# Kernel tuning notes

Measured on AMD Instinct MI355X. Metric: run time of the kernel, lower is better.

The kernel has to match this reference:

```python
import jax, jax.numpy as jnp
import numpy as np

BLOCK_N = 64  # KV tile size used by the Triton kernel (affects numerics: kernel is not exact softmax)


def _flash_fwd_buggy(q, k, v, sm_scale):
    """Faithful reproduction of the kernel's online-softmax loop.

    Note: the original kernel omits the accumulator rescaling step of true
    flash attention (acc is accumulated with the *running* denominator and
    never corrected), so we replicate that block-wise update exactly.
    q: [B,H,Sq,D], k/v: [B,H,Sk,D], Sk % BLOCK_N == 0.
    """
    B, H, Sq, D = q.shape
    Sk = k.shape[2]
    nblk = Sk // BLOCK_N
    # [nblk, B, H, BLOCK_N, D]
    kb = jnp.moveaxis(k.reshape(B, H, nblk, BLOCK_N, D), 2, 0)
    vb = jnp.moveaxis(v.reshape(B, H, nblk, BLOCK_N, D), 2, 0)

    acc0 = jnp.zeros((B, H, Sq, D), dtype=jnp.float32)
    m0 = jnp.full((B, H, Sq), -jnp.inf, dtype=jnp.float32)
    l0 = jnp.zeros((B, H, Sq), dtype=jnp.float32)

    def step(carry, kv):
        acc, m_prev, l_prev = carry
        kblk, vblk = kv  # [B,H,BLOCK_N,D]
        qk = jnp.einsum('bhmd,bhnd->bhmn', q, kblk) * sm_scale  # [B,H,Sq,BLOCK_N]
        m_curr = jnp.maximum(jnp.max(qk, axis=-1), m_prev)
        qk_exp = jnp.exp(qk - m_curr[..., None])
        l_curr = jnp.sum(qk_exp, axis=-1)
        l_new = l_prev * jnp.exp(m_prev - m_curr) + l_curr
        p = qk_exp / l_new[..., None]
        acc = acc + jnp.einsum('bhmn,bhnd->bhmd', p, vblk)
        return (acc, m_curr, l_new), None

    (acc, _, _), _ = jax.lax.scan(step, (acc0, m0, l0), (kb, vb))
    return acc


def setup_inputs() -> dict:
    key = jax.random.key(0)
    kq, kk, kv = jax.random.split(key, 3)
    B, H, S, D = 2, 16, 4096, 128
    q = jax.random.normal(kq, (B, H, S, D), dtype=jnp.float32)
    k = jax.random.normal(kk, (B, H, S, D), dtype=jnp.float32)
    v = jax.random.normal(kv, (B, H, S, D), dtype=jnp.float32)
    return {"q": q, "k": k, "v": v}


def reference(q, k, v):
    head_dim = q.shape[-1]
    sm_scale = 1.0 / np.sqrt(head_dim).astype(np.float32)
    # causal=False, dropout=0.0 (module defaults); module returns (output, None)
    return _flash_fwd_buggy(q, k, v, sm_scale)
```

## Files before the change

### kernel.cpp

```cpp
#include <hip/hip_runtime.h>
#include <hip/hip_bf16.h>
#include <math.h>


typedef __attribute__((ext_vector_type(8)))  unsigned short ushort8;
typedef __attribute__((ext_vector_type(8)))  __bf16        bf16x8;
typedef __attribute__((ext_vector_type(16))) float         f32x16;
typedef __attribute__((ext_vector_type(4)))  float         floatv4;
typedef __attribute__((ext_vector_type(2)))  unsigned int  uint2v;
typedef __attribute__((ext_vector_type(4)))  unsigned int  uint4v;

#define SQ   4096
#define SKV  4096
#define DH   128
#define BN   64
#define QB   256
#define NT   (SKV / BN)
#define KLD  136
#define VTLD 72
#define KBUF (64 * KLD)
#define VBUF (DH * VTLD)

static __device__ __forceinline__ unsigned pk2(float lo, float hi) {
    unsigned r;
    asm("v_cvt_pk_bf16_f32 %0, %1, %2" : "=v"(r) : "v"(lo), "v"(hi));
    return r;
}

__global__ __launch_bounds__(512, 2) void fa_fwd_buggy(
    const float* __restrict__ Qg, const float* __restrict__ Kg,
    const float* __restrict__ Vg, float* __restrict__ Og)
{
    __shared__ unsigned short K_lds[2 * KBUF];
    __shared__ unsigned short Vt_lds[2 * VBUF];

    const int tid  = threadIdx.x;
    const int w    = tid >> 6;
    const int lane = tid & 63;
    const int c32  = lane & 31;
    const int h    = lane >> 5;

    const int wgid  = blockIdx.x;
    const int bh    = (wgid & 7) * 4 + (wgid >> 7);
    const int qtile = (wgid >> 3) & 15;
    const int qbase = qtile * QB;
    const float qscale = 0.08838834764831845f * 1.44269504088896341f;

    const float* Qrow = Qg + ((size_t)bh * SQ + qbase + w * 32 + c32) * DH;
    ushort8 qf[8];
    #pragma unroll
    for (int ds = 0; ds < 8; ++ds) {
        floatv4 a = *(const floatv4*)(Qrow + ds * 16 + h * 8);
        floatv4 b = *(const floatv4*)(Qrow + ds * 16 + h * 8 + 4);
        uint4v u;
        u[0] = pk2(a[0]*qscale, a[1]*qscale);
        u[1] = pk2(a[2]*qscale, a[3]*qscale);
        u[2] = pk2(b[0]*qscale, b[1]*qscale);
        u[3] = pk2(b[2]*qscale, b[3]*qscale);
        qf[ds] = __builtin_bit_cast(ushort8, u);
    }

    f32x16 acc[4];
    #pragma unroll
    for (int i = 0; i < 4; ++i)
        #pragma unroll
        for (int r = 0; r < 16; ++r) acc[i][r] = 0.f;

    float l_run = 0.f;

    const float* Kbh = Kg + (size_t)bh * SKV * DH;
    const float* Vbh = Vg + (size_t)bh * SKV * DH;

    const int n_k = tid >> 3;
    const int u_k = tid & 7;
    const int dq  = tid & 31;
    const int nq  = tid >> 5;
    const int vswz = (dq >> 1) & 7;

    floatv4 ka0, ka1, kb0, kb1;
    floatv4 va0, va1, va2, va3;

#define LOAD_TILE(N0) do {                                                   \
        const float* ks_ = Kbh + (size_t)((N0) + n_k) * DH + u_k * 8;        \
        ka0 = *(const floatv4*)(ks_);        ka1 = *(const floatv4*)(ks_+4); \
        kb0 = *(const floatv4*)(ks_ + 64);   kb1 = *(const floatv4*)(ks_+68);\
        const float* vs_ = Vbh + (size_t)((N0) + nq * 4) * DH + dq * 4;      \
        va0 = *(const floatv4*)(vs_);        va1 = *(const floatv4*)(vs_+DH);\
        va2 = *(const floatv4*)(vs_+2*DH);   va3 = *(const floatv4*)(vs_+3*DH);\
    } while (0)

#define STORE_TILE(B) do {                                                   \
        unsigned short* kd_ = &K_lds[(B) * KBUF];                            \
        unsigned short* vd_ = &Vt_lds[(B) * VBUF];                           \
        uint4v u_;                                                           \
        u_[0]=pk2(ka0[0],ka0[1]); u_[1]=pk2(ka0[2],ka0[3]);                  \
        u_[2]=pk2(ka1[0],ka1[1]); u_[3]=pk2(ka1[2],ka1[3]);                  \
        *(uint4v*)&kd_[n_k * KLD + u_k * 8] = u_;                            \
        u_[0]=pk2(kb0[0],kb0[1]); u_[1]=pk2(kb0[2],kb0[3]);                  \
        u_[2]=pk2(kb1[0],kb1[1]); u_[3]=pk2(kb1[2],kb1[3]);                  \
        *(uint4v*)&kd_[n_k * KLD + (u_k + 8) * 8] = u_;                      \
        _Pragma("unroll")                                                    \
        for (int i_ = 0; i_ < 4; ++i_) {                                     \
            const int d_ = dq * 4 + i_;                                      \
            uint2v p_;                                                       \
            p_[0] = pk2(va0[i_], va1[i_]);                                   \
            p_[1] = pk2(va2[i_], va3[i_]);                                   \
            const int unit_ = (nq >> 1) ^ vswz;                              \
            *(uint2v*)&vd_[d_ * VTLD + unit_ * 8 + (nq & 1) * 4] = p_;       \
        }                                                                    \
    } while (0)

    LOAD_TILE(0);
    STORE_TILE(0);
    LOAD_TILE(BN);
    __syncthreads();

    for (int t = 0; t < NT; ++t) {
        if (t + 1 < NT) {
            STORE_TILE((t + 1) & 1);
            if (t + 2 < NT) LOAD_TILE((size_t)(t + 2) * BN);
        }
        const unsigned short* Kb = &K_lds[(t & 1) * KBUF];
        const unsigned short* Vb = &Vt_lds[(t & 1) * VBUF];

        f32x16 s[2];
        __builtin_amdgcn_s_setprio(1);
        #pragma unroll
        for (int ns = 0; ns < 2; ++ns) {
            f32x16 tt;
            #pragma unroll
            for (int r = 0; r < 16; ++r) tt[r] = 0.f;
            #pragma unroll
            for (int ds = 0; ds < 8; ++ds) {
                ushort8 kf = *(const ushort8*)&Kb[(ns * 32 + c32) * KLD + ds * 16 + h * 8];
                tt = __builtin_amdgcn_mfma_f32_32x32x16_bf16(
                        __builtin_bit_cast(bf16x8, kf),
                        __builtin_bit_cast(bf16x8, qf[ds]), tt, 0, 0, 0);
            }
            s[ns] = tt;
        }
        __builtin_amdgcn_s_setprio(0);

        float ps = 0.f;
        #pragma unroll
        for (int ns = 0; ns < 2; ++ns) {
            #pragma unroll
            for (int r = 0; r < 16; ++r)
                s[ns][r] = __builtin_amdgcn_exp2f(s[ns][r]);
            float q0 = (s[ns][0]  + s[ns][1])  + (s[ns][2]  + s[ns][3]);
            float q1 = (s[ns][4]  + s[ns][5])  + (s[ns][6]  + s[ns][7]);
            float q2 = (s[ns][8]  + s[ns][9])  + (s[ns][10] + s[ns][11]);
            float q3 = (s[ns][12] + s[ns][13]) + (s[ns][14] + s[ns][15]);
            ps += (q0 + q1) + (q2 + q3);
        }
        ps += __shfl_xor(ps, 32);
        const float ln = l_run + ps;
        l_run = ln;
        const float inv = __builtin_amdgcn_rcpf(ln);

        unsigned wrd[2][8];
        #pragma unroll
        for (int ns = 0; ns < 2; ++ns)
            #pragma unroll
            for (int i = 0; i < 8; ++i)
                wrd[ns][i] = pk2(s[ns][2*i] * inv, s[ns][2*i+1] * inv);

        ushort8 pa[4];
        #pragma unroll
        for (int step = 0; step < 4; ++step) {
            const int ns   = step >> 1;
            const int base = 4 * (step & 1);
            auto rA = __builtin_amdgcn_permlane32_swap(
                          (int)wrd[ns][base + 0], (int)wrd[ns][base + 2], false, false);
            auto rB = __builtin_amdgcn_permlane32_swap(
                          (int)wrd[ns][base + 1], (int)wrd[ns][base + 3], false, false);
            uint4v pw;
            pw[0] = (unsigned)rA[0];
            pw[1] = (unsigned)rB[0];
            pw[2] = (unsigned)rA[1];
            pw[3] = (unsigned)rB[1];
            pa[step] = __builtin_bit_cast(ushort8, pw);
        }

        __builtin_amdgcn_s_setprio(1);
        #pragma unroll
        for (int dt = 0; dt < 4; ++dt) {
            const int d  = dt * 32 + c32;
            const int fz = (d >> 3) & 7;
            #pragma unroll
            for (int step = 0; step < 4; ++step) {
                ushort8 vb = *(const ushort8*)&Vb[d * VTLD + (((2*step + h) ^ fz) * 8)];
                acc[dt] = __builtin_amdgcn_mfma_f32_32x32x16_bf16(
                    __builtin_bit_cast(bf16x8, pa[step]),
                    __builtin_bit_cast(bf16x8, vb), acc[dt], 0, 0, 0);
            }
        }
        __builtin_amdgcn_s_setprio(0);

        __syncthreads();
    }

    float* ob = Og + ((size_t)bh * SQ + qbase + w * 32) * DH + c32;
    #pragma unroll
    for (int dt = 0; dt < 4; ++dt) {
        #pragma unroll
        for (int r = 0; r < 16; ++r) {
            const int qrow = (r & 3) + 8 * (r >> 2) + 4 * h;
            ob[(size_t)qrow * DH + dt * 32] = acc[dt][r];
        }
    }
}

extern "C" void kernel_launch(void* const* d_in, const int* in_sizes, int n_in,
                              void* d_out, int out_size, void* d_ws, size_t ws_size,
                              hipStream_t stream) {
    const float* q = (const float*)d_in[0];
    const float* k = (const float*)d_in[1];
    const float* v = (const float*)d_in[2];
    float* o = (float*)d_out;
    dim3 grid((SQ / QB) * 32);
    fa_fwd_buggy<<<grid, 512, 0, stream>>>(q, k, v, o);
}
```

Before: 298.8 us.

## Software-pipeline QK of next tile with softmax/PV of current tile

```diff
diff --git a/kernel.cpp b/kernel.cpp
--- a/kernel.cpp
+++ b/kernel.cpp
@@ -32,7 +32,7 @@
     const float* __restrict__ Vg, float* __restrict__ Og)
 {
     __shared__ unsigned short K_lds[2 * KBUF];
-    __shared__ unsigned short Vt_lds[2 * VBUF];
+    __shared__ unsigned short Vt_lds[3 * VBUF];
 
     const int tid  = threadIdx.x;
     const int w    = tid >> 6;
@@ -89,9 +89,9 @@
         va2 = *(const floatv4*)(vs_+2*DH);   va3 = *(const floatv4*)(vs_+3*DH);\
     } while (0)
 
-#define STORE_TILE(B) do {                                                   \
-        unsigned short* kd_ = &K_lds[(B) * KBUF];                            \
-        unsigned short* vd_ = &Vt_lds[(B) * VBUF];                           \
+#define STORE_TILE(KS, VS) do {                                              \
+        unsigned short* kd_ = &K_lds[(KS) * KBUF];                           \
+        unsigned short* vd_ = &Vt_lds[(VS) * VBUF];                          \
         uint4v u_;                                                           \
         u_[0]=pk2(ka0[0],ka0[1]); u_[1]=pk2(ka0[2],ka0[3]);                  \
         u_[2]=pk2(ka1[0],ka1[1]); u_[3]=pk2(ka1[2],ka1[3]);                  \
@@ -110,94 +110,126 @@
         }                                                                    \
     } while (0)
 
+#define QK_TILE(S0, S1, KS) do {                                             \
+        const unsigned short* kb_ = &K_lds[(KS) * KBUF];                     \
+        f32x16 t0_, t1_;                                                     \
+        _Pragma("unroll")                                                    \
+        for (int r_ = 0; r_ < 16; ++r_) { t0_[r_] = 0.f; t1_[r_] = 0.f; }    \
+        __builtin_amdgcn_s_setprio(1);                                       \
+        _Pragma("unroll")                                                    \
+        for (int ds_ = 0; ds_ < 8; ++ds_) {                                  \
+            ushort8 kf0_ = *(const ushort8*)&kb_[(c32)      * KLD + ds_*16 + h*8]; \
+            ushort8 kf1_ = *(const ushort8*)&kb_[(32 + c32) * KLD + ds_*16 + h*8]; \
+            t0_ = __builtin_amdgcn_mfma_f32_32x32x16_bf16(                   \
+                    __builtin_bit_cast(bf16x8, kf0_),                        \
+                    __builtin_bit_cast(bf16x8, qf[ds_]), t0_, 0, 0, 0);      \
+            t1_ = __builtin_amdgcn_mfma_f32_32x32x16_bf16(                   \
+                    __builtin_bit_cast(bf16x8, kf1_),                        \
+                    __builtin_bit_cast(bf16x8, qf[ds_]), t1_, 0, 0, 0);      \
+        }                                                                    \
+        __builtin_amdgcn_s_setprio(0);                                       \
+        S0 = t0_; S1 = t1_;                                                  \
+    } while (0)
+
+#define SM_PACK(S0, S1, PA) do {                                             \
+        float ps_ = 0.f;                                                     \
+        _Pragma("unroll")                                                    \
+        for (int r_ = 0; r_ < 16; ++r_) S0[r_] = __builtin_amdgcn_exp2f(S0[r_]); \
+        _Pragma("unroll")                                                    \
+        for (int r_ = 0; r_ < 16; ++r_) S1[r_] = __builtin_amdgcn_exp2f(S1[r_]); \
+        {                                                                    \
+            float q0_ = (S0[0]+S0[1])+(S0[2]+S0[3]);                         \
+            float q1_ = (S0[4]+S0[5])+(S0[6]+S0[7]);                         \
+            float q2_ = (S0[8]+S0[9])+(S0[10]+S0[11]);                       \
+            float q3_ = (S0[12]+S0[13])+(S0[14]+S0[15]);                     \
+            float q4_ = (S1[0]+S1[1])+(S1[2]+S1[3]);                         \
+            float q5_ = (S1[4]+S1[5])+(S1[6]+S1[7]);                         \
+            float q6_ = (S1[8]+S1[9])+(S1[10]+S1[11]);                       \
+            float q7_ = (S1[12]+S1[13])+(S1[14]+S1[15]);                     \
+            ps_ = ((q0_+q1_)+(q2_+q3_)) + ((q4_+q5_)+(q6_+q7_));             \
+        }                                                                    \
+        ps_ += __shfl_xor(ps_, 32);                                          \
+        const float ln_ = l_run + ps_;                                       \
+        l_run = ln_;                                                         \
+        const float inv_ = __builtin_amdgcn_rcpf(ln_);                       \
+        unsigned wrd_[2][8];                                                 \
+        _Pragma("unroll")                                                    \
+        for (int i_ = 0; i_ < 8; ++i_)                                       \
+            wrd_[0][i_] = pk2(S0[2*i_] * inv_, S0[2*i_+1] * inv_);           \
+        _Pragma("unroll")                                                    \
+        for (int i_ = 0; i_ < 8; ++i_)                                       \
+            wrd_[1][i_] = pk2(S1[2*i_] * inv_, S1[2*i_+1] * inv_);           \
+        _Pragma("unroll")                                                    \
+        for (int st_ = 0; st_ < 4; ++st_) {                                  \
+            const int ns_   = st_ >> 1;                                      \
+            const int base_ = 4 * (st_ & 1);                                 \
+            auto rA_ = __builtin_amdgcn_permlane32_swap(                     \
+                          (int)wrd_[ns_][base_ + 0], (int)wrd_[ns_][base_ + 2], false, false); \
+            auto rB_ = __builtin_amdgcn_permlane32_swap(                     \
+                          (int)wrd_[ns_][base_ + 1], (int)wrd_[ns_][base_ + 3], false, false); \
+            uint4v pw_;                                                      \
+            pw_[0] = (unsigned)rA_[0];                                       \
+            pw_[1] = (unsigned)rB_[0];                                       \
+            pw_[2] = (unsigned)rA_[1];                                       \
+            pw_[3] = (unsigned)rB_[1];                                       \
+            PA[st_] = __builtin_bit_cast(ushort8, pw_);                      \
+        }                                                                    \
+    } while (0)
+
+#define PV_TILE(PA, VS) do {                                                 \
+        const unsigned short* vb_ = &Vt_lds[(VS) * VBUF];                    \
+        __builtin_amdgcn_s_setprio(1);                                       \
+        _Pragma("unroll")                                                    \
+        for (int dt_ = 0; dt_ < 4; ++dt_) {                                  \
+            const int d_  = dt_ * 32 + c32;                                  \
+            const int fz_ = (d_ >> 3) & 7;                                   \
+            _Pragma("unroll")                                                \
+            for (int st_ = 0; st_ < 4; ++st_) {                              \
+                ushort8 vv_ = *(const ushort8*)&vb_[d_ * VTLD + (((2*st_ + h) ^ fz_) * 8)]; \
+                acc[dt_] = __builtin_amdgcn_mfma_f32_32x32x16_bf16(          \
+                    __builtin_bit_cast(bf16x8, PA[st_]),                     \
+                    __builtin_bit_cast(bf16x8, vv_), acc[dt_], 0, 0, 0);     \
+            }                                                                \
+        }                                                                    \
+        __builtin_amdgcn_s_setprio(0);                                       \
+    } while (0)
+
     LOAD_TILE(0);
-    STORE_TILE(0);
+    STORE_TILE(0, 0);
     LOAD_TILE(BN);
     __syncthreads();
 
-    for (int t = 0; t < NT; ++t) {
-        if (t + 1 < NT) {
-            STORE_TILE((t + 1) & 1);
-            if (t + 2 < NT) LOAD_TILE((size_t)(t + 2) * BN);
-        }
-        const unsigned short* Kb = &K_lds[(t & 1) * KBUF];
-        const unsigned short* Vb = &Vt_lds[(t & 1) * VBUF];
-
-        f32x16 s[2];
-        __builtin_amdgcn_s_setprio(1);
-        #pragma unroll
-        for (int ns = 0; ns < 2; ++ns) {
-            f32x16 tt;
-            #pragma unroll
-            for (int r = 0; r < 16; ++r) tt[r] = 0.f;
-            #pragma unroll
-            for (int ds = 0; ds < 8; ++ds) {
-                ushort8 kf = *(const ushort8*)&Kb[(ns * 32 + c32) * KLD + ds * 16 + h * 8];
-                tt = __builtin_amdgcn_mfma_f32_32x32x16_bf16(
-                        __builtin_bit_cast(bf16x8, kf),
-                        __builtin_bit_cast(bf16x8, qf[ds]), tt, 0, 0, 0);
-            }
-            s[ns] = tt;
-        }
-        __builtin_amdgcn_s_setprio(0);
-
-        float ps = 0.f;
-        #pragma unroll
-        for (int ns = 0; ns < 2; ++ns) {
-            #pragma unroll
-            for (int r = 0; r < 16; ++r)
-                s[ns][r] = __builtin_amdgcn_exp2f(s[ns][r]);
-            float q0 = (s[ns][0]  + s[ns][1])  + (s[ns][2]  + s[ns][3]);
-            float q1 = (s[ns][4]  + s[ns][5])  + (s[ns][6]  + s[ns][7]);
-            float q2 = (s[ns][8]  + s[ns][9])  + (s[ns][10] + s[ns][11]);
-            float q3 = (s[ns][12] + s[ns][13]) + (s[ns][14] + s[ns][15]);
-            ps += (q0 + q1) + (q2 + q3);
-        }
-        ps += __shfl_xor(ps, 32);
-        const float ln = l_run + ps;
-        l_run = ln;
-        const float inv = __builtin_amdgcn_rcpf(ln);
-
-        unsigned wrd[2][8];
-        #pragma unroll
-        for (int ns = 0; ns < 2; ++ns)
-            #pragma unroll
-            for (int i = 0; i < 8; ++i)
-                wrd[ns][i] = pk2(s[ns][2*i] * inv, s[ns][2*i+1] * inv);
-
-        ushort8 pa[4];
-        #pragma unroll
-        for (int step = 0; step < 4; ++step) {
-            const int ns   = step >> 1;
-            const int base = 4 * (step & 1);
-            auto rA = __builtin_amdgcn_permlane32_swap(
-                          (int)wrd[ns][base + 0], (int)wrd[ns][base + 2], false, false);
-            auto rB = __builtin_amdgcn_permlane32_swap(
-                          (int)wrd[ns][base + 1], (int)wrd[ns][base + 3], false, false);
-            uint4v pw;
-            pw[0] = (unsigned)rA[0];
-            pw[1] = (unsigned)rB[0];
-            pw[2] = (unsigned)rA[1];
-            pw[3] = (unsigned)rB[1];
-            pa[step] = __builtin_bit_cast(ushort8, pw);
-        }
-
-        __builtin_amdgcn_s_setprio(1);
-        #pragma unroll
-        for (int dt = 0; dt < 4; ++dt) {
-            const int d  = dt * 32 + c32;
-            const int fz = (d >> 3) & 7;
-            #pragma unroll
-            for (int step = 0; step < 4; ++step) {
-                ushort8 vb = *(const ushort8*)&Vb[d * VTLD + (((2*step + h) ^ fz) * 8)];
-                acc[dt] = __builtin_amdgcn_mfma_f32_32x32x16_bf16(
-                    __builtin_bit_cast(bf16x8, pa[step]),
-                    __builtin_bit_cast(bf16x8, vb), acc[dt], 0, 0, 0);
-            }
-        }
-        __builtin_amdgcn_s_setprio(0);
-
+    f32x16 sA0, sA1, sB0, sB1;
+    QK_TILE(sA0, sA1, 0);
+
+    int vs0 = 0;
+    for (int t = 0; t < NT; t += 2) {
+        const int vs1 = (vs0 == 2) ? 0 : vs0 + 1;
+        const int vs2 = (vs1 == 2) ? 0 : vs1 + 1;
+
+        STORE_TILE(1, vs1);
+        if (t + 2 < NT) LOAD_TILE((size_t)(t + 2) * BN);
         __syncthreads();
+        QK_TILE(sB0, sB1, 1);
+        {
+            ushort8 pa[4];
+            SM_PACK(sA0, sA1, pa);
+            PV_TILE(pa, vs0);
+        }
+
+        if (t + 2 < NT) {
+            STORE_TILE(0, vs2);
+            if (t + 3 < NT) LOAD_TILE((size_t)(t + 3) * BN);
+        }
+        __syncthreads();
+        if (t + 2 < NT) QK_TILE(sA0, sA1, 0);
+        {
+            ushort8 pa[4];
+            SM_PACK(sB0, sB1, pa);
+            PV_TILE(pa, vs1);
+        }
+
+        vs0 = vs2;
     }
 
     float* ob = Og + ((size_t)bh * SQ + qbase + w * 32) * DH + c32;
```

New measurement: 296.6 us. No clear change (-0.7%).

## Halve workgroup to 4 waves and pack exp scores to bf16 before normalizing

Applied to the files above, without the earlier changes.

```diff
diff --git a/kernel.cpp b/kernel.cpp
--- a/kernel.cpp
+++ b/kernel.cpp
@@ -14,7 +14,7 @@
 #define SKV  4096
 #define DH   128
 #define BN   64
-#define QB   256
+#define QB   128
 #define NT   (SKV / BN)
 #define KLD  136
 #define VTLD 72
@@ -27,7 +27,7 @@
     return r;
 }
 
-__global__ __launch_bounds__(512, 2) void fa_fwd_buggy(
+__global__ __launch_bounds__(256, 2) void fa_fwd_buggy(
     const float* __restrict__ Qg, const float* __restrict__ Kg,
     const float* __restrict__ Vg, float* __restrict__ Og)
 {
@@ -41,8 +41,8 @@
     const int h    = lane >> 5;
 
     const int wgid  = blockIdx.x;
-    const int bh    = (wgid & 7) * 4 + (wgid >> 7);
-    const int qtile = (wgid >> 3) & 15;
+    const int bh    = (wgid & 7) * 4 + (wgid >> 8);
+    const int qtile = (wgid >> 3) & 31;
     const int qbase = qtile * QB;
     const float qscale = 0.08838834764831845f * 1.44269504088896341f;
 
@@ -71,22 +71,26 @@
     const float* Kbh = Kg + (size_t)bh * SKV * DH;
     const float* Vbh = Vg + (size_t)bh * SKV * DH;
 
-    const int n_k = tid >> 3;
-    const int u_k = tid & 7;
+    const int n_k = tid >> 2;
+    const int u_k = tid & 3;
+    const int nq  = tid >> 5;
     const int dq  = tid & 31;
-    const int nq  = tid >> 5;
     const int vswz = (dq >> 1) & 7;
 
-    floatv4 ka0, ka1, kb0, kb1;
-    floatv4 va0, va1, va2, va3;
+    floatv4 ka0, ka1, kb0, kb1, kc0, kc1, ke0, ke1;
+    floatv4 va0, va1, va2, va3, va4, va5, va6, va7;
 
 #define LOAD_TILE(N0) do {                                                   \
         const float* ks_ = Kbh + (size_t)((N0) + n_k) * DH + u_k * 8;        \
-        ka0 = *(const floatv4*)(ks_);        ka1 = *(const floatv4*)(ks_+4); \
-        kb0 = *(const floatv4*)(ks_ + 64);   kb1 = *(const floatv4*)(ks_+68);\
-        const float* vs_ = Vbh + (size_t)((N0) + nq * 4) * DH + dq * 4;      \
+        ka0 = *(const floatv4*)(ks_);      ka1 = *(const floatv4*)(ks_+4);   \
+        kb0 = *(const floatv4*)(ks_+32);   kb1 = *(const floatv4*)(ks_+36);  \
+        kc0 = *(const floatv4*)(ks_+64);   kc1 = *(const floatv4*)(ks_+68);  \
+        ke0 = *(const floatv4*)(ks_+96);   ke1 = *(const floatv4*)(ks_+100); \
+        const float* vs_ = Vbh + (size_t)((N0) + nq * 8) * DH + dq * 4;      \
         va0 = *(const floatv4*)(vs_);        va1 = *(const floatv4*)(vs_+DH);\
         va2 = *(const floatv4*)(vs_+2*DH);   va3 = *(const floatv4*)(vs_+3*DH);\
+        va4 = *(const floatv4*)(vs_+4*DH);   va5 = *(const floatv4*)(vs_+5*DH);\
+        va6 = *(const floatv4*)(vs_+6*DH);   va7 = *(const floatv4*)(vs_+7*DH);\
     } while (0)
 
 #define STORE_TILE(B) do {                                                   \
@@ -98,15 +102,23 @@
         *(uint4v*)&kd_[n_k * KLD + u_k * 8] = u_;                            \
         u_[0]=pk2(kb0[0],kb0[1]); u_[1]=pk2(kb0[2],kb0[3]);                  \
         u_[2]=pk2(kb1[0],kb1[1]); u_[3]=pk2(kb1[2],kb1[3]);                  \
+        *(uint4v*)&kd_[n_k * KLD + (u_k + 4) * 8] = u_;                      \
+        u_[0]=pk2(kc0[0],kc0[1]); u_[1]=pk2(kc0[2],kc0[3]);                  \
+        u_[2]=pk2(kc1[0],kc1[1]); u_[3]=pk2(kc1[2],kc1[3]);                  \
         *(uint4v*)&kd_[n_k * KLD + (u_k + 8) * 8] = u_;                      \
+        u_[0]=pk2(ke0[0],ke0[1]); u_[1]=pk2(ke0[2],ke0[3]);                  \
+        u_[2]=pk2(ke1[0],ke1[1]); u_[3]=pk2(ke1[2],ke1[3]);                  \
+        *(uint4v*)&kd_[n_k * KLD + (u_k + 12) * 8] = u_;                     \
         _Pragma("unroll")                                                    \
         for (int i_ = 0; i_ < 4; ++i_) {                                     \
             const int d_ = dq * 4 + i_;                                      \
             uint2v p_;                                                       \
             p_[0] = pk2(va0[i_], va1[i_]);                                   \
             p_[1] = pk2(va2[i_], va3[i_]);                                   \
-            const int unit_ = (nq >> 1) ^ vswz;                              \
-            *(uint2v*)&vd_[d_ * VTLD + unit_ * 8 + (nq & 1) * 4] = p_;       \
+            *(uint2v*)&vd_[d_ * VTLD + (nq ^ vswz) * 8] = p_;                \
+            p_[0] = pk2(va4[i_], va5[i_]);                                   \
+            p_[1] = pk2(va6[i_], va7[i_]);                                   \
+            *(uint2v*)&vd_[d_ * VTLD + (nq ^ vswz) * 8 + 4] = p_;            \
         }                                                                    \
     } while (0)
 
@@ -123,57 +135,56 @@
         const unsigned short* Kb = &K_lds[(t & 1) * KBUF];
         const unsigned short* Vb = &Vt_lds[(t & 1) * VBUF];
 
-        f32x16 s[2];
-        __builtin_amdgcn_s_setprio(1);
+        unsigned wrdU[2][8];
+        float psn[2];
         #pragma unroll
         for (int ns = 0; ns < 2; ++ns) {
-            f32x16 tt;
-            #pragma unroll
-            for (int r = 0; r < 16; ++r) tt[r] = 0.f;
+            f32x16 s;
+            #pragma unroll
+            for (int r = 0; r < 16; ++r) s[r] = 0.f;
+            __builtin_amdgcn_s_setprio(1);
             #pragma unroll
             for (int ds = 0; ds < 8; ++ds) {
                 ushort8 kf = *(const ushort8*)&Kb[(ns * 32 + c32) * KLD + ds * 16 + h * 8];
-                tt = __builtin_amdgcn_mfma_f32_32x32x16_bf16(
+                s = __builtin_amdgcn_mfma_f32_32x32x16_bf16(
                         __builtin_bit_cast(bf16x8, kf),
-                        __builtin_bit_cast(bf16x8, qf[ds]), tt, 0, 0, 0);
+                        __builtin_bit_cast(bf16x8, qf[ds]), s, 0, 0, 0);
             }
-            s[ns] = tt;
-        }
-        __builtin_amdgcn_s_setprio(0);
-
-        float ps = 0.f;
-        #pragma unroll
-        for (int ns = 0; ns < 2; ++ns) {
+            __builtin_amdgcn_s_setprio(0);
             #pragma unroll
             for (int r = 0; r < 16; ++r)
-                s[ns][r] = __builtin_amdgcn_exp2f(s[ns][r]);
-            float q0 = (s[ns][0]  + s[ns][1])  + (s[ns][2]  + s[ns][3]);
-            float q1 = (s[ns][4]  + s[ns][5])  + (s[ns][6]  + s[ns][7]);
-            float q2 = (s[ns][8]  + s[ns][9])  + (s[ns][10] + s[ns][11]);
-            float q3 = (s[ns][12] + s[ns][13]) + (s[ns][14] + s[ns][15]);
-            ps += (q0 + q1) + (q2 + q3);
-        }
+                s[r] = __builtin_amdgcn_exp2f(s[r]);
+            float q0 = (s[0]  + s[1])  + (s[2]  + s[3]);
+            float q1 = (s[4]  + s[5])  + (s[6]  + s[7]);
+            float q2 = (s[8]  + s[9])  + (s[10] + s[11]);
+            float q3 = (s[12] + s[13]) + (s[14] + s[15]);
+            psn[ns] = (q0 + q1) + (q2 + q3);
+            #pragma unroll
+            for (int i = 0; i < 8; ++i)
+                wrdU[ns][i] = pk2(s[2*i], s[2*i+1]);
+        }
+
+        float ps = psn[0] + psn[1];
         ps += __shfl_xor(ps, 32);
         const float ln = l_run + ps;
         l_run = ln;
         const float inv = __builtin_amdgcn_rcpf(ln);
 
-        unsigned wrd[2][8];
-        #pragma unroll
-        for (int ns = 0; ns < 2; ++ns)
-            #pragma unroll
-            for (int i = 0; i < 8; ++i)
-                wrd[ns][i] = pk2(s[ns][2*i] * inv, s[ns][2*i+1] * inv);
-
         ushort8 pa[4];
         #pragma unroll
         for (int step = 0; step < 4; ++step) {
             const int ns   = step >> 1;
             const int base = 4 * (step & 1);
-            auto rA = __builtin_amdgcn_permlane32_swap(
-                          (int)wrd[ns][base + 0], (int)wrd[ns][base + 2], false, false);
-            auto rB = __builtin_amdgcn_permlane32_swap(
-                          (int)wrd[ns][base + 1], (int)wrd[ns][base + 3], false, false);
+            unsigned ws[4];
+            #pragma unroll
+            for (int k = 0; k < 4; ++k) {
+                const unsigned uw = wrdU[ns][base + k];
+                float lo = __builtin_bit_cast(float, uw << 16);
+                float hi = __builtin_bit_cast(float, uw & 0xffff0000u);
+                ws[k] = pk2(lo * inv, hi * inv);
+            }
+            auto rA = __builtin_amdgcn_permlane32_swap((int)ws[0], (int)ws[2], false, false);
+            auto rB = __builtin_amdgcn_permlane32_swap((int)ws[1], (int)ws[3], false, false);
             uint4v pw;
             pw[0] = (unsigned)rA[0];
             pw[1] = (unsigned)rB[0];
@@ -219,5 +230,5 @@
     const float* v = (const float*)d_in[2];
     float* o = (float*)d_out;
     dim3 grid((SQ / QB) * 32);
-    fa_fwd_buggy<<<grid, 512, 0, stream>>>(q, k, v, o);
+    fa_fwd_buggy<<<grid, 256, 0, stream>>>(q, k, v, o);
 }
```

New measurement: 346.9 us. 1.16x slower.
